# Kernel tuning notes

Hardware: AMD Instinct MI355X
Metric: run time of the kernel (lower is better)

The kernel has to match this reference:

```python
import jax, jax.numpy as jnp
import numpy as np

BITS = 8
STEP = 2.0 ** (-5)
QMIN = -2.0 ** (BITS - 1)
QMAX = 2.0 ** (BITS - 1) - 1


def _q(x):
    # DFXP fixed-point fake-quantize: clamp(round(x/step), qmin, qmax)*step
    return jnp.clip(jnp.round(x / STEP), QMIN, QMAX) * STEP


@jax.custom_vjp
def fq(x):
    # ForwardQuantizer: quantize in fwd, straight-through grad
    return _q(x)

def _fq_fwd(x):
    return _q(x), None

def _fq_bwd(_, g):
    return (g,)

fq.defvjp(_fq_fwd, _fq_bwd)


def gq(x):
    # BackwardQuantizer: identity in forward (grad quantized only in bwd pass)
    return x


def setup_inputs() -> dict:
    key = jax.random.key(0)
    ks = jax.random.split(key, 5)
    B, I, H = 2048, 1024, 1024
    return {
        "X": jax.random.normal(ks[0], (B, I), dtype=jnp.float32),
        "h": jax.random.normal(ks[1], (B, H), dtype=jnp.float32),
        "c": jax.random.normal(ks[2], (B, H), dtype=jnp.float32),
        "weight": jax.random.normal(ks[3], (4 * H, I + H), dtype=jnp.float32) * (H ** -0.5),
        "bias": jax.random.normal(ks[4], (4 * H,), dtype=jnp.float32) * (H ** -0.5),
    }


def reference(X, h, c, weight, bias):
    # concat + input/weight/bias fake-quant
    Xh = fq(jnp.concatenate([X, h], axis=1))          # [B, I+H]
    Wq = fq(weight)                                    # [4H, I+H]
    bq = fq(bias)                                      # [4H]
    y = gq(Xh @ Wq.T + bq)                             # [B, 4H]
    i, f, g, o = jnp.split(y, 4, axis=1)
    i = fq(gq(jax.nn.sigmoid(i)))
    f = fq(gq(jax.nn.sigmoid(f)))
    g = fq(gq(jnp.tanh(g)))
    o = fq(gq(jax.nn.sigmoid(o)))
    cq = fq(c)
    c_new = gq(cq * f) + gq(i * g)
    cell_tanh = fq(gq(jnp.tanh(c_new)))
    h_new = gq(cell_tanh * o)
    return (h_new, c_new)
```

## Files before the change

kernel.cpp:

```cpp
#include <hip/hip_runtime.h>
#include <stdint.h>

#define B_DIM 2048
#define K_DIM 2048
#define N_PACK 4096

typedef int v4i __attribute__((ext_vector_type(4)));

__device__ __forceinline__ float fqf(float x) {
    float q = rintf(x * 32.0f);
    q = fminf(fmaxf(q, -128.0f), 127.0f);
    return q * 0.03125f;
}
__device__ __forceinline__ int q8i(float x) {
    float q = rintf(x * 32.0f);
    q = fminf(fmaxf(q, -128.0f), 127.0f);
    return (int)q;
}
__device__ __forceinline__ float fsigm(float x) {
    return __fdividef(1.0f, 1.0f + __expf(-x));
}
__device__ __forceinline__ float ftanh(float x) {
    return __fdividef(2.0f, 1.0f + __expf(-2.0f * x)) - 1.0f;
}

__global__ __launch_bounds__(256) void quant_pack(
    const float* __restrict__ X, const float* __restrict__ hI,
    const float* __restrict__ W, const float* __restrict__ bias,
    int8_t* __restrict__ Xhq, int8_t* __restrict__ Wq, float* __restrict__ bqp)
{
    const int bid = blockIdx.x;
    const int t = threadIdx.x;
    if (bid < B_DIM) {
        const int m = bid;
        const int k0 = t * 8;
        const float* src = (k0 < 1024) ? (X + (size_t)m * 1024 + k0)
                                       : (hI + (size_t)m * 1024 + (k0 - 1024));
        float4 v0 = *(const float4*)src;
        float4 v1 = *(const float4*)(src + 4);
        union { int8_t c[8]; int64_t ll; } u;
        u.c[0] = (int8_t)q8i(v0.x); u.c[1] = (int8_t)q8i(v0.y);
        u.c[2] = (int8_t)q8i(v0.z); u.c[3] = (int8_t)q8i(v0.w);
        u.c[4] = (int8_t)q8i(v1.x); u.c[5] = (int8_t)q8i(v1.y);
        u.c[6] = (int8_t)q8i(v1.z); u.c[7] = (int8_t)q8i(v1.w);
        *(int64_t*)(Xhq + (size_t)m * K_DIM + k0) = u.ll;
    } else if (bid < B_DIM + N_PACK) {
        const int r = bid - B_DIM;
        const int gate = r >> 10, j = r & 1023;
        const int p = (j << 2) | gate;
        const int k0 = t * 8;
        const float* src = W + (size_t)r * K_DIM + k0;
        float4 v0 = *(const float4*)src;
        float4 v1 = *(const float4*)(src + 4);
        union { int8_t c[8]; int64_t ll; } u;
        u.c[0] = (int8_t)q8i(v0.x); u.c[1] = (int8_t)q8i(v0.y);
        u.c[2] = (int8_t)q8i(v0.z); u.c[3] = (int8_t)q8i(v0.w);
        u.c[4] = (int8_t)q8i(v1.x); u.c[5] = (int8_t)q8i(v1.y);
        u.c[6] = (int8_t)q8i(v1.z); u.c[7] = (int8_t)q8i(v1.w);
        *(int64_t*)(Wq + (size_t)p * K_DIM + k0) = u.ll;
    } else {
        for (int idx = t; idx < N_PACK; idx += 256) {
            const int gate = idx >> 10, j = idx & 1023;
            bqp[(j << 2) | gate] = fqf(bias[idx]);
        }
    }
}

__global__ __launch_bounds__(256, 2) void lstm_gemm(
    const int8_t* __restrict__ Xhq, const int8_t* __restrict__ Wq,
    const float* __restrict__ bqp, const float* __restrict__ cin,
    float* __restrict__ hout, float* __restrict__ cout_)
{
    __shared__ __align__(16) char raw[65536];
    const int t = threadIdx.x;
    const int l = t & 63;
    const int wave = t >> 6;
    const int wm = wave >> 1;
    const int wn = wave & 1;

    const int b = blockIdx.x;
    const int xcd = b & 7;
    const int slot = b >> 3;
    const int mt = ((xcd & 1) << 3) + (slot & 7);
    const int nt = ((xcd >> 1) << 3) + (slot >> 3);
    const int m0 = mt * 128;
    const int n0 = nt * 128;

    v4i acc[4][4];
    #pragma unroll
    for (int i = 0; i < 4; ++i)
        #pragma unroll
        for (int j = 0; j < 4; ++j)
            acc[i][j] = (v4i)0;

    const int srow = t >> 3;
    const int schunk = (t & 7) ^ (srow & 7);
    const int8_t* gA = Xhq + (size_t)(m0 + srow) * K_DIM + schunk * 16;
    const int8_t* gB = Wq  + (size_t)(n0 + srow) * K_DIM + schunk * 16;

#define STAGE(p, kt) do { \
    char* Ad_ = raw + (p) * 32768; \
    char* Bd_ = raw + (p) * 32768 + 16384; \
    _Pragma("unroll") \
    for (int i_ = 0; i_ < 4; ++i_) { \
        __builtin_amdgcn_global_load_lds( \
            (const __attribute__((address_space(1))) uint32_t*)(gA + (size_t)(i_ * 32) * K_DIM + (kt) * 128), \
            (__attribute__((address_space(3))) uint32_t*)(Ad_ + i_ * 4096 + t * 16), 16, 0, 0); \
        __builtin_amdgcn_global_load_lds( \
            (const __attribute__((address_space(1))) uint32_t*)(gB + (size_t)(i_ * 32) * K_DIM + (kt) * 128), \
            (__attribute__((address_space(3))) uint32_t*)(Bd_ + i_ * 4096 + t * 16), 16, 0, 0); \
    } \
} while (0)

    STAGE(0, 0);

    const int rrow = l & 15;
    const int lx = l & 7;
    const int g4 = l >> 4;

    for (int kt = 0; kt < 16; ++kt) {
        const int p = kt & 1;
        if (kt < 15) {
            STAGE(p ^ 1, kt + 1);
            asm volatile("s_waitcnt vmcnt(8)" ::: "memory");
        } else {
            asm volatile("s_waitcnt vmcnt(0)" ::: "memory");
        }
        asm volatile("s_barrier" ::: "memory");

        const char* As = raw + p * 32768;
        const char* Bs = raw + p * 32768 + 16384;
        v4i a[2][4], b2[2][4];
        #pragma unroll
        for (int kk = 0; kk < 2; ++kk) {
            const int c = kk * 4 + g4;
            const int sl = (c ^ lx) * 16;
            #pragma unroll
            for (int mf = 0; mf < 4; ++mf) {
                const int r = wm * 64 + mf * 16 + rrow;
                a[kk][mf] = *(const v4i*)(As + r * 128 + sl);
            }
            #pragma unroll
            for (int nf = 0; nf < 4; ++nf) {
                const int r = wn * 64 + nf * 16 + rrow;
                b2[kk][nf] = *(const v4i*)(Bs + r * 128 + sl);
            }
        }
        #pragma unroll
        for (int kk = 0; kk < 2; ++kk)
            #pragma unroll
            for (int mf = 0; mf < 4; ++mf)
                #pragma unroll
                for (int nf = 0; nf < 4; ++nf)
                    acc[mf][nf] = __builtin_amdgcn_mfma_i32_16x16x64_i8(
                        a[kk][mf], b2[kk][nf], acc[mf][nf], 0, 0, 0);
        asm volatile("s_waitcnt lgkmcnt(0)" ::: "memory");
        asm volatile("s_barrier" ::: "memory");
    }

#undef STAGE

    float (*Cs)[132] = (float(*)[132])raw;
    const float sc = 0.0009765625f;
    for (int half = 0; half < 2; ++half) {
        __syncthreads();
        if (wm == half) {
            #pragma unroll
            for (int mf = 0; mf < 4; ++mf) {
                const int rb = mf * 16 + ((l >> 4) << 2);
                #pragma unroll
                for (int nf = 0; nf < 4; ++nf) {
                    const int col = wn * 64 + nf * 16 + (l & 15);
                    #pragma unroll
                    for (int rr = 0; rr < 4; ++rr)
                        Cs[rb + rr][col] = (float)acc[mf][nf][rr] * sc;
                }
            }
        }
        __syncthreads();
        #pragma unroll
        for (int it = 0; it < 8; ++it) {
            const int idx = it * 256 + t;
            const int row = idx >> 5;
            const int jl = idx & 31;
            float4 y = *(const float4*)&Cs[row][jl << 2];
            float4 bb = *(const float4*)&bqp[n0 + (jl << 2)];
            const int m = m0 + half * 64 + row;
            const int j = (n0 >> 2) + jl;
            const float ig = fqf(fsigm(y.x + bb.x));
            const float fg = fqf(fsigm(y.y + bb.y));
            const float gg = fqf(ftanh(y.z + bb.z));
            const float og = fqf(fsigm(y.w + bb.w));
            const float cq = fqf(cin[(size_t)m * 1024 + j]);
            const float cn = cq * fg + ig * gg;
            const float hn = fqf(ftanh(cn)) * og;
            hout[(size_t)m * 1024 + j] = hn;
            cout_[(size_t)m * 1024 + j] = cn;
        }
    }
}

extern "C" void kernel_launch(void* const* d_in, const int* in_sizes, int n_in,
                              void* d_out, int out_size, void* d_ws, size_t ws_size,
                              hipStream_t stream) {
    const float* X    = (const float*)d_in[0];
    const float* h    = (const float*)d_in[1];
    const float* c    = (const float*)d_in[2];
    const float* W    = (const float*)d_in[3];
    const float* bias = (const float*)d_in[4];

    float* out   = (float*)d_out;
    float* h_out = out;
    float* c_out = out + (size_t)B_DIM * 1024;

    char* ws = (char*)d_ws;
    int8_t* Xhq = (int8_t*)ws;
    int8_t* Wq  = (int8_t*)(ws + (size_t)4 * 1024 * 1024);
    float*  bqp = (float*)(ws + (size_t)12 * 1024 * 1024);

    quant_pack<<<B_DIM + N_PACK + 1, 256, 0, stream>>>(X, h, W, bias, Xhq, Wq, bqp);

    lstm_gemm<<<512, 256, 0, stream>>>(Xhq, Wq, bqp, c, h_out, c_out);
}
```

Baseline: 42.40 us.

## Enlarge GEMM tile to 128x256 with 8 waves and triple-buffered LDS

```diff
diff --git a/kernel.cpp b/kernel.cpp
--- a/kernel.cpp
+++ b/kernel.cpp
@@ -66,25 +66,25 @@
     }
 }
 
-__global__ __launch_bounds__(256, 2) void lstm_gemm(
+__global__ __launch_bounds__(512, 1) void lstm_gemm(
     const int8_t* __restrict__ Xhq, const int8_t* __restrict__ Wq,
     const float* __restrict__ bqp, const float* __restrict__ cin,
     float* __restrict__ hout, float* __restrict__ cout_)
 {
-    __shared__ __align__(16) char raw[65536];
+    __shared__ __align__(16) char raw[147456];
     const int t = threadIdx.x;
     const int l = t & 63;
     const int wave = t >> 6;
-    const int wm = wave >> 1;
-    const int wn = wave & 1;
+    const int wm = wave >> 2;
+    const int wn = wave & 3;
 
     const int b = blockIdx.x;
     const int xcd = b & 7;
     const int slot = b >> 3;
     const int mt = ((xcd & 1) << 3) + (slot & 7);
-    const int nt = ((xcd >> 1) << 3) + (slot >> 3);
+    const int nt = ((xcd >> 1) << 2) + (slot >> 3);
     const int m0 = mt * 128;
-    const int n0 = nt * 128;
+    const int n0 = nt * 256;
 
     v4i acc[4][4];
     #pragma unroll
@@ -98,54 +98,50 @@
     const int8_t* gA = Xhq + (size_t)(m0 + srow) * K_DIM + schunk * 16;
     const int8_t* gB = Wq  + (size_t)(n0 + srow) * K_DIM + schunk * 16;
 
-#define STAGE(p, kt) do { \
-    char* Ad_ = raw + (p) * 32768; \
-    char* Bd_ = raw + (p) * 32768 + 16384; \
+#define STAGE(sb, kt) do { \
+    char* Ad_ = raw + (sb); \
+    char* Bd_ = raw + (sb) + 16384; \
     _Pragma("unroll") \
-    for (int i_ = 0; i_ < 4; ++i_) { \
+    for (int i_ = 0; i_ < 2; ++i_) \
         __builtin_amdgcn_global_load_lds( \
-            (const __attribute__((address_space(1))) uint32_t*)(gA + (size_t)(i_ * 32) * K_DIM + (kt) * 128), \
-            (__attribute__((address_space(3))) uint32_t*)(Ad_ + i_ * 4096 + t * 16), 16, 0, 0); \
+            (const __attribute__((address_space(1))) uint32_t*)(gA + (size_t)(i_ * 64) * K_DIM + (kt) * 128), \
+            (__attribute__((address_space(3))) uint32_t*)(Ad_ + i_ * 8192 + t * 16), 16, 0, 0); \
+    _Pragma("unroll") \
+    for (int i_ = 0; i_ < 4; ++i_) \
         __builtin_amdgcn_global_load_lds( \
-            (const __attribute__((address_space(1))) uint32_t*)(gB + (size_t)(i_ * 32) * K_DIM + (kt) * 128), \
-            (__attribute__((address_space(3))) uint32_t*)(Bd_ + i_ * 4096 + t * 16), 16, 0, 0); \
-    } \
+            (const __attribute__((address_space(1))) uint32_t*)(gB + (size_t)(i_ * 64) * K_DIM + (kt) * 128), \
+            (__attribute__((address_space(3))) uint32_t*)(Bd_ + i_ * 8192 + t * 16), 16, 0, 0); \
 } while (0)
 
     STAGE(0, 0);
+    STAGE(49152, 1);
 
     const int rrow = l & 15;
     const int lx = l & 7;
     const int g4 = l >> 4;
 
+    int sCur = 0;
+    int sNxt = 98304;
     for (int kt = 0; kt < 16; ++kt) {
-        const int p = kt & 1;
-        if (kt < 15) {
-            STAGE(p ^ 1, kt + 1);
-            asm volatile("s_waitcnt vmcnt(8)" ::: "memory");
-        } else {
-            asm volatile("s_waitcnt vmcnt(0)" ::: "memory");
-        }
+        if (kt < 15) asm volatile("s_waitcnt vmcnt(6)" ::: "memory");
+        else         asm volatile("s_waitcnt vmcnt(0)" ::: "memory");
         asm volatile("s_barrier" ::: "memory");
-
-        const char* As = raw + p * 32768;
-        const char* Bs = raw + p * 32768 + 16384;
+        if (kt < 14) STAGE(sNxt, kt + 2);
+
+        const char* As = raw + sCur;
+        const char* Bs = As + 16384;
         v4i a[2][4], b2[2][4];
         #pragma unroll
         for (int kk = 0; kk < 2; ++kk) {
-            const int c = kk * 4 + g4;
-            const int sl = (c ^ lx) * 16;
-            #pragma unroll
-            for (int mf = 0; mf < 4; ++mf) {
-                const int r = wm * 64 + mf * 16 + rrow;
-                a[kk][mf] = *(const v4i*)(As + r * 128 + sl);
-            }
-            #pragma unroll
-            for (int nf = 0; nf < 4; ++nf) {
-                const int r = wn * 64 + nf * 16 + rrow;
-                b2[kk][nf] = *(const v4i*)(Bs + r * 128 + sl);
-            }
-        }
+            const int sl = ((kk * 4 + g4) ^ lx) * 16;
+            #pragma unroll
+            for (int mf = 0; mf < 4; ++mf)
+                a[kk][mf] = *(const v4i*)(As + (wm * 64 + mf * 16 + rrow) * 128 + sl);
+            #pragma unroll
+            for (int nf = 0; nf < 4; ++nf)
+                b2[kk][nf] = *(const v4i*)(Bs + (wn * 64 + nf * 16 + rrow) * 128 + sl);
+        }
+        __builtin_amdgcn_s_setprio(1);
         #pragma unroll
         for (int kk = 0; kk < 2; ++kk)
             #pragma unroll
@@ -154,20 +150,23 @@
                 for (int nf = 0; nf < 4; ++nf)
                     acc[mf][nf] = __builtin_amdgcn_mfma_i32_16x16x64_i8(
                         a[kk][mf], b2[kk][nf], acc[mf][nf], 0, 0, 0);
-        asm volatile("s_waitcnt lgkmcnt(0)" ::: "memory");
-        asm volatile("s_barrier" ::: "memory");
+        __builtin_amdgcn_s_setprio(0);
+
+        sCur += 49152; if (sCur == 147456) sCur = 0;
+        sNxt += 49152; if (sNxt == 147456) sNxt = 0;
     }
 
 #undef STAGE
 
-    float (*Cs)[132] = (float(*)[132])raw;
+    float (*Cs)[264] = (float(*)[264])raw;
     const float sc = 0.0009765625f;
-    for (int half = 0; half < 2; ++half) {
+    for (int q = 0; q < 4; ++q) {
         __syncthreads();
-        if (wm == half) {
-            #pragma unroll
-            for (int mf = 0; mf < 4; ++mf) {
-                const int rb = mf * 16 + ((l >> 4) << 2);
+        if (wm == (q >> 1)) {
+            #pragma unroll
+            for (int mf2 = 0; mf2 < 2; ++mf2) {
+                const int mf = (q & 1) * 2 + mf2;
+                const int rb = mf2 * 16 + ((l >> 4) << 2);
                 #pragma unroll
                 for (int nf = 0; nf < 4; ++nf) {
                     const int col = wn * 64 + nf * 16 + (l & 15);
@@ -179,18 +178,18 @@
         }
         __syncthreads();
         #pragma unroll
-        for (int it = 0; it < 8; ++it) {
-            const int idx = it * 256 + t;
-            const int row = idx >> 5;
-            const int jl = idx & 31;
+        for (int it = 0; it < 4; ++it) {
+            const int idx = it * 512 + t;
+            const int row = idx >> 6;
+            const int jl = idx & 63;
             float4 y = *(const float4*)&Cs[row][jl << 2];
-            float4 bb = *(const float4*)&bqp[n0 + (jl << 2)];
-            const int m = m0 + half * 64 + row;
+            float4 bv = *(const float4*)&bqp[n0 + (jl << 2)];
+            const int m = m0 + q * 32 + row;
             const int j = (n0 >> 2) + jl;
-            const float ig = fqf(fsigm(y.x + bb.x));
-            const float fg = fqf(fsigm(y.y + bb.y));
-            const float gg = fqf(ftanh(y.z + bb.z));
-            const float og = fqf(fsigm(y.w + bb.w));
+            const float ig = fqf(fsigm(y.x + bv.x));
+            const float fg = fqf(fsigm(y.y + bv.y));
+            const float gg = fqf(ftanh(y.z + bv.z));
+            const float og = fqf(fsigm(y.w + bv.w));
             const float cq = fqf(cin[(size_t)m * 1024 + j]);
             const float cn = cq * fg + ig * gg;
             const float hn = fqf(ftanh(cn)) * og;
@@ -220,5 +219,5 @@
 
     quant_pack<<<B_DIM + N_PACK + 1, 256, 0, stream>>>(X, h, W, bias, Xhq, Wq, bqp);
 
-    lstm_gemm<<<512, 256, 0, stream>>>(Xhq, Wq, bqp, c, h_out, c_out);
-}
+    lstm_gemm<<<256, 512, 0, stream>>>(Xhq, Wq, bqp, c, h_out, c_out);
+}
```

Measured after the change: 60.16 us. +41.9%, slower.
